# Performance work log

Measured on AMD Instinct MI355X. Metric: run time of the kernel, lower is better.

## Reference

```python
import jax, jax.numpy as jnp
import numpy as np

NUM_HEADS = 8
EMBED_DIM = 512
EXPAND = 3
RPE_DIM = 512
RPE_LAYERS = 3
B, N = 4, 2048
D1 = (EXPAND * EMBED_DIM) // NUM_HEADS * NUM_HEADS  # 1536
HEAD_DIM = D1 // NUM_HEADS  # 192


def srms(x):
    # SimpleRMSNorm: x / (||x||_2 * d^{-1/2} + eps)
    d = x.shape[-1]
    rms = jnp.linalg.norm(x, axis=-1, keepdims=True) * (d ** -0.5)
    return x / (rms + 1e-8)


def rpe_net(idx, Wp, bp, Wl, bl, Wr, br):
    # idx: (m, 1) relative positions -> (m, h*head_dim)
    h = idx @ Wp.T + bp
    for i in range(Wl.shape[0]):  # fixed small layer count
        h = jax.nn.relu(srms(h)) @ Wl[i].T + bl[i]
    return jax.nn.relu(srms(h)) @ Wr.T + br


def setup_inputs() -> dict:
    key = jax.random.key(0)
    ks = jax.random.split(key, 12)
    s = 0.02
    return {
        "x": jax.random.normal(ks[0], (B, N, EMBED_DIM), jnp.float32),
        "Wu": jax.random.normal(ks[1], (D1, EMBED_DIM), jnp.float32) * s,
        "bu": jnp.zeros((D1,), jnp.float32),
        "Wv": jax.random.normal(ks[2], (D1, EMBED_DIM), jnp.float32) * s,
        "bv": jnp.zeros((D1,), jnp.float32),
        "Wo": jax.random.normal(ks[3], (EMBED_DIM, D1), jnp.float32) * s,
        "bo": jnp.zeros((EMBED_DIM,), jnp.float32),
        "Wp": jax.random.normal(ks[4], (RPE_DIM, 1), jnp.float32) * s,
        "bp": jax.random.normal(ks[5], (RPE_DIM,), jnp.float32) * s,
        "Wl": jax.random.normal(ks[6], (RPE_LAYERS, RPE_DIM, RPE_DIM), jnp.float32) * s,
        "bl": jax.random.normal(ks[7], (RPE_LAYERS, RPE_DIM), jnp.float32) * s,
        "Wr": jax.random.normal(ks[8], (NUM_HEADS * HEAD_DIM, RPE_DIM), jnp.float32) * s,
        "br": jax.random.normal(ks[9], (NUM_HEADS * HEAD_DIM,), jnp.float32) * s,
    }


def reference(x, Wu, bu, Wv, bv, Wo, bo, Wp, bp, Wl, bl, Wr, br):
    b, n, e = x.shape
    d1 = Wu.shape[0]
    hd = d1 // NUM_HEADS
    u = jax.nn.silu(x @ Wu.T + bu)                       # (b, n, d1)
    v = jax.nn.silu(x @ Wv.T + bv)                       # (b, n, d1)
    v = v.reshape(b, n, NUM_HEADS, hd).transpose(0, 2, 1, 3)  # (b, h, n, d)
    # Tno non-causal, par_type=1: indices [0, 1..n-1, 0, -(n-1)..-1]
    pos = jnp.arange(1, n, dtype=x.dtype)
    zero = jnp.zeros((1,), x.dtype)
    idx = jnp.concatenate([zero, pos, zero, -pos[::-1]])[:, None]  # (2n, 1)
    a = rpe_net(idx, Wp, bp, Wl, bl, Wr, br)             # (2n, h*d)
    a = a.reshape(2 * n, NUM_HEADS, hd).transpose(1, 0, 2)  # (h, 2n, d)
    m = 2 * n
    # circular conv of length 2n along sequence, truncate to n
    y = jnp.fft.rfft(v, m, axis=2) * jnp.fft.rfft(a, m, axis=1)[None]
    out = jnp.fft.irfft(y, m, axis=2)[:, :, :n, :]       # (b, h, n, d)
    out = out.transpose(0, 2, 1, 3).reshape(b, n, d1)    # (b, n, d1)
    return (u * out) @ Wo.T + bo
```

## Files before the change

### kernel.cpp

```cpp
#include <hip/hip_runtime.h>

#define N_SEQ 2048
#define M_FFT 4096
#define D1    1536
#define NH    8
#define HD    192
#define ED    512

typedef __bf16 bf16;
typedef __bf16 bf16x4 __attribute__((ext_vector_type(4)));
typedef __bf16 bf16x8 __attribute__((ext_vector_type(8)));
typedef float  floatx4 __attribute__((ext_vector_type(4)));
typedef float  cx __attribute__((ext_vector_type(2)));

enum { MODE_PLAIN = 0, MODE_SILU_UV = 1, MODE_AT = 3, MODE_RPE = 4 };

__device__ __forceinline__ void gload16(const void* g, void* l) {
    __builtin_amdgcn_global_load_lds(
        (const __attribute__((address_space(1))) void*)g,
        (__attribute__((address_space(3))) void*)l, 16, 0, 0);
}

template<int MODE, typename OutT>
__global__ __launch_bounds__(256) void gemm_bf16(
    const bf16* __restrict__ A, const bf16* __restrict__ Bw,
    const float* __restrict__ bias, const float* __restrict__ bias2,
    OutT* __restrict__ C, OutT* __restrict__ C2,
    int M, int Nc, int K,
    const float* __restrict__ scale_in, float* __restrict__ sumsq_out)
{
    __shared__ __align__(16) bf16 As[128 * 32];
    __shared__ __align__(16) bf16 Bs[128 * 32];

    const int tid  = threadIdx.x;
    const int row0 = blockIdx.y * 128;
    const int col0 = blockIdx.x * 128;
    const int wid  = tid >> 6;
    const int lane = tid & 63;
    const int lm   = lane & 15;
    const int lk   = lane >> 4;
    const int wm   = wid >> 1;
    const int wn   = wid & 1;
    const int ldrow  = tid >> 2;
    const int ldcol8 = (tid & 3) * 8;

    floatx4 acc[4][4] = {};

    const bf16* Ag = A  + ((size_t)(row0 + ldrow)) * K + ldcol8;
    const bf16* Bg = Bw + ((size_t)(col0 + ldrow)) * K + ldcol8;
    bf16* AsW = As + (wid * 16) * 32;
    bf16* BsW = Bs + (wid * 16) * 32;

    for (int k0 = 0; k0 < K; k0 += 32) {
        gload16(Ag + k0, AsW);
        gload16(Ag + (size_t)64 * K + k0, AsW + 64 * 32);
        gload16(Bg + k0, BsW);
        gload16(Bg + (size_t)64 * K + k0, BsW + 64 * 32);
        __syncthreads();

        bf16x8 af[4], bfr[4];
        #pragma unroll
        for (int mi = 0; mi < 4; ++mi)
            af[mi] = *(const bf16x8*)&As[(wm * 64 + mi * 16 + lm) * 32 + lk * 8];
        #pragma unroll
        for (int nj = 0; nj < 4; ++nj)
            bfr[nj] = *(const bf16x8*)&Bs[(wn * 64 + nj * 16 + lm) * 32 + lk * 8];
        #pragma unroll
        for (int mi = 0; mi < 4; ++mi)
            #pragma unroll
            for (int nj = 0; nj < 4; ++nj)
                acc[mi][nj] = __builtin_amdgcn_mfma_f32_16x16x32_bf16(
                    af[mi], bfr[nj], acc[mi][nj], 0, 0, 0);
        __syncthreads();
    }

    const float* bs = bias;
    OutT* dst = C;
    int cadj = 0;
    if (MODE == MODE_SILU_UV && col0 >= D1) { bs = bias2; dst = C2; cadj = D1; }

    float bcol[4];
    #pragma unroll
    for (int nj = 0; nj < 4; ++nj)
        bcol[nj] = bs[col0 - cadj + wn * 64 + nj * 16 + lm];

    if (MODE == MODE_RPE) {
        #pragma unroll
        for (int mi = 0; mi < 4; ++mi) {
            #pragma unroll
            for (int r = 0; r < 4; ++r) {
                const int row = row0 + wm * 64 + mi * 16 + lk * 4 + r;
                float sc = 1.0f;
                if (scale_in)
                    sc = 1.0f / (sqrtf(scale_in[row]) * 0.04419417382415922f + 1e-8f);
                float ssq = 0.0f;
                #pragma unroll
                for (int nj = 0; nj < 4; ++nj) {
                    const int col = col0 + wn * 64 + nj * 16 + lm;
                    float val = acc[mi][nj][r] * sc + bcol[nj];
                    ssq += val * val;
                    ((bf16*)C)[(size_t)row * Nc + col] = (bf16)fmaxf(val, 0.0f);
                }
                ssq += __shfl_xor(ssq, 1, 64);
                ssq += __shfl_xor(ssq, 2, 64);
                ssq += __shfl_xor(ssq, 4, 64);
                ssq += __shfl_xor(ssq, 8, 64);
                if (lm == 0) atomicAdd(&sumsq_out[row], ssq);
            }
        }
        return;
    }

    #pragma unroll
    for (int mi = 0; mi < 4; ++mi) {
        const int rbase = row0 + wm * 64 + mi * 16 + lk * 4;
        float sc[4];
        #pragma unroll
        for (int r = 0; r < 4; ++r) {
            sc[r] = 1.0f;
            if (MODE == MODE_AT && scale_in)
                sc[r] = 1.0f / (sqrtf(scale_in[rbase + r]) * 0.04419417382415922f + 1e-8f);
        }
        #pragma unroll
        for (int nj = 0; nj < 4; ++nj) {
            const int col = col0 - cadj + wn * 64 + nj * 16 + lm;
            float vals[4];
            #pragma unroll
            for (int r = 0; r < 4; ++r) {
                float val = acc[mi][nj][r] * sc[r] + bcol[nj];
                if (MODE == MODE_SILU_UV)
                    val = val / (1.0f + __expf(-val));
                vals[r] = val;
            }
            if (MODE == MODE_SILU_UV) {
                int b = rbase >> 11, s = rbase & 2047;
                bf16x4 o;
                #pragma unroll
                for (int r = 0; r < 4; ++r) o[r] = (bf16)vals[r];
                *(bf16x4*)&((bf16*)dst)[((size_t)(b * D1 + col)) * N_SEQ + s] = o;
            } else if (MODE == MODE_AT) {
                float4 o = make_float4(vals[0], vals[1], vals[2], vals[3]);
                *(float4*)&((float*)C)[(size_t)col * M + rbase] = o;
            } else {
                #pragma unroll
                for (int r = 0; r < 4; ++r)
                    C[(size_t)(rbase + r) * Nc + col] = (OutT)vals[r];
            }
        }
    }
}

__global__ __launch_bounds__(256) void f2b_all_kernel(
    const float* __restrict__ x,  const float* __restrict__ s0,
    const float* __restrict__ s1, const float* __restrict__ s2,
    const float* __restrict__ s3, const float* __restrict__ s4,
    const float* __restrict__ Wp, const float* __restrict__ bp,
    bf16* __restrict__ x_bf, bf16* __restrict__ w_bf,
    float* __restrict__ sumsq, bf16* __restrict__ g0)
{
    const int bid = blockIdx.x;
    const int tid = threadIdx.x;
    __shared__ float red[4];

    if (bid < 7936) {
        const float* src;
        bf16* dst;
        size_t off;
        if (bid < 4096) {
            src = x; dst = x_bf; off = (size_t)bid * 1024;
        } else {
            int t = bid - 4096;
            int seg = t / 768;
            src = seg == 0 ? s0 : seg == 1 ? s1 : seg == 2 ? s2
                : seg == 3 ? s3 : s4;
            dst = w_bf + (size_t)seg * 786432;
            off = (size_t)(t % 768) * 1024;
        }
        size_t i = off + (size_t)tid * 4;
        float4 f = *(const float4*)(src + i);
        union { bf16 h[4]; short4 s; } u4;
        u4.h[0] = (bf16)f.x; u4.h[1] = (bf16)f.y;
        u4.h[2] = (bf16)f.z; u4.h[3] = (bf16)f.w;
        *(short4*)(dst + i) = u4.s;
    } else if (bid < 7948) {
        size_t i = (size_t)(bid - 7936) * 1024 + (size_t)tid * 4;
        *(float4*)(sumsq + i) = make_float4(0.f, 0.f, 0.f, 0.f);
    } else {
        const int j = bid - 7948;
        float idxv = (j < N_SEQ) ? (float)j
                                 : (j == N_SEQ ? 0.0f : (float)(j - 2 * N_SEQ));
        float h1 = idxv * Wp[tid] + bp[tid];
        float h2 = idxv * Wp[tid + 256] + bp[tid + 256];
        float ss = h1 * h1 + h2 * h2;
        #pragma unroll
        for (int off = 32; off > 0; off >>= 1) ss += __shfl_down(ss, off, 64);
        if ((tid & 63) == 0) red[tid >> 6] = ss;
        __syncthreads();
        float tot = red[0] + red[1] + red[2] + red[3];
        float scale = 1.0f / (sqrtf(tot) * 0.04419417382415922f + 1e-8f);
        g0[(size_t)j * ED + tid]       = (bf16)fmaxf(h1 * scale, 0.0f);
        g0[(size_t)j * ED + tid + 256] = (bf16)fmaxf(h2 * scale, 0.0f);
    }
}

#define FFT_LDS_SZ 4381
#define CC1 0.9238795325112867f
#define SS1 0.3826834323650898f
#define RR2 0.7071067811865476f

__device__ __forceinline__ int fpad(int i) { return i + (i >> 4) + 2 * (i >> 8); }

__device__ __forceinline__ cx mkcx(float a, float b) { cx r; r.x = a; r.y = b; return r; }
__device__ __forceinline__ cx cmul(cx a, cx b) {
    cx br = mkcx(-b.y, b.x);
    return a.xx * b + a.yy * br;
}
__device__ __forceinline__ cx cneg_i(cx a) { return mkcx(a.y, -a.x); }
__device__ __forceinline__ cx cpos_i(cx a) { return mkcx(-a.y, a.x); }
__host__ __device__ constexpr int brev4(int t) {
    return ((t & 1) << 3) | ((t & 2) << 1) | ((t & 4) >> 1) | ((t & 8) >> 3);
}

template<bool HZ>
__device__ __forceinline__ void fft16_dif_r4(cx x[16]) {
    const cx W1 = mkcx( CC1, -SS1);
    const cx W2 = mkcx( RR2, -RR2);
    const cx W3 = mkcx( SS1, -CC1);
    const cx W6 = mkcx(-RR2, -RR2);
    const cx W9 = mkcx(-CC1,  SS1);
    #pragma unroll
    for (int n = 0; n < 4; ++n) {
        cx A, B, C, D;
        if (HZ) { A = x[n]; C = x[n]; B = x[n + 4]; D = x[n + 4]; }
        else {
            A = x[n] + x[n + 8];      C = x[n] - x[n + 8];
            B = x[n + 4] + x[n + 12]; D = x[n + 4] - x[n + 12];
        }
        cx s = A - B;
        cx nid = cneg_i(D);
        cx m = C + nid;
        cx p = C - nid;
        x[n] = A + B;
        if (n == 0)      { x[4] = s;            x[8]  = m;           x[12] = p; }
        else if (n == 1) { x[5] = cmul(s, W2);  x[9]  = cmul(m, W1); x[13] = cmul(p, W3); }
        else if (n == 2) { x[6] = cneg_i(s);    x[10] = cmul(m, W2); x[14] = cmul(p, W6); }
        else             { x[7] = cmul(s, W6);  x[11] = cmul(m, W3); x[15] = cmul(p, W9); }
    }
    #pragma unroll
    for (int q = 0; q < 16; q += 4) {
        cx a = x[q], b = x[q + 1], c = x[q + 2], d = x[q + 3];
        cx a1 = a + c, c1 = a - c;
        cx b1 = b + d, d1 = cneg_i(b - d);
        x[q]     = a1 + b1;
        x[q + 1] = a1 - b1;
        x[q + 2] = c1 + d1;
        x[q + 3] = c1 - d1;
    }
}

template<bool HALF_OUT>
__device__ __forceinline__ void fft16_dit_inv_r4(cx x[16]) {
    const cx V1 = mkcx( CC1, SS1);
    const cx V2 = mkcx( RR2, RR2);
    const cx V3 = mkcx( SS1, CC1);
    const cx V6 = mkcx(-RR2, RR2);
    #pragma unroll
    for (int q = 0; q < 16; q += 4) {
        cx a = x[q], b = x[q + 1], c = x[q + 2], d = x[q + 3];
        cx a1 = a + b, b1 = a - b;
        cx c1 = c + d, d1 = c - d;
        cx t = cpos_i(d1);
        x[q]     = a1 + c1;
        x[q + 2] = a1 - c1;
        x[q + 1] = b1 + t;
        x[q + 3] = b1 - t;
    }
    #pragma unroll
    for (int n = 0; n < 4; ++n) {
        cx t1, t2;
        if (n == 0)      { t1 = x[4];             t2 = x[12]; }
        else if (n == 1) { t1 = cmul(x[5],  V2);  t2 = cmul(x[13], V2); }
        else if (n == 2) { t1 = cpos_i(x[6]);     t2 = cpos_i(x[14]); }
        else             { t1 = cmul(x[7],  V6);  t2 = cmul(x[15], V6); }
        cx P = x[n] + t1, Q = x[n] - t1;
        cx R = x[n + 8] + t2, S = x[n + 8] - t2;
        cx t, u;
        if (n == 0)      { t = R;            u = S; }
        else if (n == 1) { t = cmul(R, V1);  u = cmul(S, V1); }
        else if (n == 2) { t = cmul(R, V2);  u = cmul(S, V2); }
        else             { t = cmul(R, V3);  u = cmul(S, V3); }
        cx iu = cpos_i(u);
        x[n]     = P + t;
        x[n + 4] = Q + iu;
        if (!HALF_OUT) {
            x[n + 8]  = P - t;
            x[n + 12] = Q - iu;
        }
    }
}

__device__ __forceinline__ void stage_twiddle_tree(
    cx v[16], int j, float rden, float sgn)
{
    float s, c;
    __sincosf(sgn * 6.283185307179586f * (float)j * rden, &s, &c);
    cx w[16];
    w[1] = mkcx(c, s);
    w[2] = cmul(w[1], w[1]);
    w[3] = cmul(w[1], w[2]);
    w[4] = cmul(w[2], w[2]);
    w[5] = cmul(w[1], w[4]);
    w[6] = cmul(w[2], w[4]);
    w[7] = cmul(w[3], w[4]);
    w[8] = cmul(w[4], w[4]);
    #pragma unroll
    for (int t = 9; t < 16; ++t) w[t] = cmul(w[t - 8], w[8]);
    #pragma unroll
    for (int tau = 1; tau < 16; ++tau)
        v[brev4(tau)] = cmul(v[brev4(tau)], w[tau]);
}

template<bool HALF_ZERO>
__device__ void fft4096_fwd(cx* d, int tid)
{
    cx v[16];
    {
        const int j = tid;
        if (HALF_ZERO) {
            #pragma unroll
            for (int t = 0; t < 8; ++t) v[t] = d[fpad(j + (t << 8))];
            fft16_dif_r4<true>(v);
        } else {
            #pragma unroll
            for (int t = 0; t < 16; ++t) v[t] = d[fpad(j + (t << 8))];
            fft16_dif_r4<false>(v);
        }
        stage_twiddle_tree(v, j, 1.0f / 4096.0f, -1.0f);
        #pragma unroll
        for (int p = 0; p < 16; ++p) d[fpad(j + (p << 8))] = v[p];
    }
    __syncthreads();
    {
        const int base = ((tid >> 4) << 8) + (tid & 15);
        #pragma unroll
        for (int t = 0; t < 16; ++t) v[t] = d[fpad(base + (t << 4))];
        fft16_dif_r4<false>(v);
        stage_twiddle_tree(v, tid & 15, 1.0f / 256.0f, -1.0f);
        #pragma unroll
        for (int p = 0; p < 16; ++p) d[fpad(base + (p << 4))] = v[p];
    }
    __syncthreads();
    {
        const int base = tid << 4;
        #pragma unroll
        for (int t = 0; t < 16; ++t) v[t] = d[fpad(base + t)];
        fft16_dif_r4<false>(v);
        #pragma unroll
        for (int p = 0; p < 16; ++p) d[fpad(base + p)] = v[p];
    }
    __syncthreads();
}

__global__ __launch_bounds__(256) void fft_a_kernel(
    const float* __restrict__ a_t, cx* __restrict__ Wspec)
{
    __shared__ cx data[FFT_LDS_SZ];
    const int tid = threadIdx.x;
    const int h = blockIdx.x / 96, dp = blockIdx.x % 96;

    const float* r0 = a_t + ((size_t)(h * HD + 2 * dp)) * M_FFT;
    const float* r1 = r0 + M_FFT;

    for (int j = tid; j < 4096; j += 256) data[fpad(j)] = mkcx(r0[j], r1[j]);
    __syncthreads();
    fft4096_fwd<false>(data, tid);

    cx* outrow = Wspec + (size_t)blockIdx.x * 4096;
    for (int j = tid; j < 4096; j += 256) outrow[j] = data[fpad(j)];
}

__global__ __launch_bounds__(256) void fft_conv_kernel(
    const bf16* __restrict__ v_t, const cx* __restrict__ Wspec,
    const bf16* __restrict__ u_t, bf16* __restrict__ gated_t)
{
    __shared__ cx data[FFT_LDS_SZ];
    const int tid = threadIdx.x;
    const int bx = blockIdx.x;
    const int b  = bx / 768;
    const int r  = bx % 768;
    const int h  = r / 96, dp = r % 96;
    const int ch = h * HD + 2 * dp;

    const bf16* z0 = v_t + ((size_t)(b * D1 + ch)) * N_SEQ;
    const bf16* z1 = z0 + N_SEQ;

    {
        const int s = tid * 8;
        bf16x8 a0 = *(const bf16x8*)(z0 + s);
        bf16x8 a1 = *(const bf16x8*)(z1 + s);
        #pragma unroll
        for (int i = 0; i < 8; ++i)
            data[fpad(s + i)] = mkcx((float)a0[i], (float)a1[i]);
    }
    __syncthreads();

    fft4096_fwd<true>(data, tid);

    const cx* Wrow = Wspec + (size_t)r * 4096;
    cx v[16];
    {
        const int base = tid << 4;
        #pragma unroll
        for (int i = 0; i < 16; ++i) {
            const int p  = base + i;
            const int k  = __brev((unsigned)p) >> 20;
            const int km = (4096 - k) & 4095;
            const int p2 = __brev((unsigned)km) >> 20;
            cx Zk = data[fpad(p)];
            cx Zm = data[fpad(p2)];
            cx Wk = Wrow[p];
            cx Wm = Wrow[p2];
            cx V0 = 0.5f * (Zk + mkcx(Zm.x, -Zm.y));
            cx V1 = 0.5f * (mkcx(Zk.y, -Zk.x) + mkcx(Zm.y, Zm.x));
            cx A0 = 0.5f * (Wk + mkcx(Wm.x, -Wm.y));
            cx A1 = 0.5f * (mkcx(Wk.y, -Wk.x) + mkcx(Wm.y, Wm.x));
            cx P = cmul(V0, A0), Q = cmul(V1, A1);
            v[i] = P + cpos_i(Q);
        }
        __syncthreads();
        fft16_dit_inv_r4<false>(v);
        #pragma unroll
        for (int i = 0; i < 16; ++i) data[fpad(base + i)] = v[i];
    }
    __syncthreads();
    {
        const int base = ((tid >> 4) << 8) + (tid & 15);
        #pragma unroll
        for (int p = 0; p < 16; ++p) v[p] = data[fpad(base + (p << 4))];
        stage_twiddle_tree(v, tid & 15, 1.0f / 256.0f, 1.0f);
        fft16_dit_inv_r4<false>(v);
        #pragma unroll
        for (int t = 0; t < 16; ++t) data[fpad(base + (t << 4))] = v[t];
    }
    __syncthreads();
    {
        const int j = tid;
        #pragma unroll
        for (int p = 0; p < 16; ++p) v[p] = data[fpad(j + (p << 8))];
        stage_twiddle_tree(v, j, 1.0f / 4096.0f, 1.0f);
        fft16_dit_inv_r4<true>(v);
        #pragma unroll
        for (int t = 0; t < 8; ++t) data[fpad(j + (t << 8))] = v[t];
    }
    __syncthreads();

    const float inv_m = 1.0f / 4096.0f;
    const bf16* u0 = u_t + ((size_t)(b * D1 + ch)) * N_SEQ;
    const bf16* u1 = u0 + N_SEQ;
    bf16* g0 = gated_t + ((size_t)(b * D1 + ch)) * N_SEQ;
    bf16* g1 = g0 + N_SEQ;
    {
        const int t = tid * 8;
        bf16x8 ua = *(const bf16x8*)(u0 + t);
        bf16x8 ub = *(const bf16x8*)(u1 + t);
        bf16x8 oa, ob;
        #pragma unroll
        for (int i = 0; i < 8; ++i) {
            cx y = data[fpad(t + i)];
            oa[i] = (bf16)(y.x * inv_m * (float)ua[i]);
            ob[i] = (bf16)(y.y * inv_m * (float)ub[i]);
        }
        *(bf16x8*)(g0 + t) = oa;
        *(bf16x8*)(g1 + t) = ob;
    }
}

__global__ __launch_bounds__(256) void transpose_cs_kernel(
    const bf16* __restrict__ in, bf16* __restrict__ outp)
{
    __shared__ bf16 tile[64 * 68];
    const int c0 = blockIdx.x * 64;
    const int m0 = blockIdx.y * 64;
    const int b  = m0 >> 11;
    const int s0 = m0 & 2047;
    const int tid = threadIdx.x;
    const int cl = tid >> 4;
    const int sc = (tid & 15) * 4;
    #pragma unroll
    for (int p = 0; p < 4; ++p) {
        int c = p * 16 + cl;
        bf16x4 v = *(const bf16x4*)&in[((size_t)(b * D1 + c0 + c)) * N_SEQ + s0 + sc];
        *(bf16x4*)&tile[c * 68 + sc] = v;
    }
    __syncthreads();
    const int sl = tid >> 4;
    const int cc = (tid & 15) * 4;
    #pragma unroll
    for (int p = 0; p < 4; ++p) {
        int s = p * 16 + sl;
        bf16x4 o;
        #pragma unroll
        for (int j = 0; j < 4; ++j) o[j] = tile[(cc + j) * 68 + s];
        *(bf16x4*)&outp[((size_t)(m0 + s)) * D1 + c0 + cc] = o;
    }
}

extern "C" void kernel_launch(void* const* d_in, const int* in_sizes, int n_in,
                              void* d_out, int out_size, void* d_ws, size_t ws_size,
                              hipStream_t stream)
{
    const float* x  = (const float*)d_in[0];
    const float* Wu = (const float*)d_in[1];
    const float* bu = (const float*)d_in[2];
    const float* Wv = (const float*)d_in[3];
    const float* bv = (const float*)d_in[4];
    const float* Wo = (const float*)d_in[5];
    const float* bo = (const float*)d_in[6];
    const float* Wp = (const float*)d_in[7];
    const float* bp = (const float*)d_in[8];
    const float* Wl = (const float*)d_in[9];
    const float* bl = (const float*)d_in[10];
    const float* Wr = (const float*)d_in[11];
    const float* br = (const float*)d_in[12];
    float* out = (float*)d_out;

    float* ws      = (float*)d_ws;
    float* a_t     = ws;
    float* Wspec   = a_t   + 6291456;
    float* sumsq   = Wspec + 6291456;
    bf16*  bfws    = (bf16*)(sumsq + 12288);
    bf16*  x_bf    = bfws;
    bf16*  w_bf    = x_bf    + 4194304;
    bf16*  Wuv_bf  = w_bf;
    bf16*  Wo_bf   = w_bf    + 2 * 786432;
    bf16*  Wl_bf   = Wo_bf   + 786432;
    bf16*  Wr_bf   = Wl_bf   + 786432;
    bf16*  gA      = Wr_bf   + 786432;
    bf16*  gB      = gA      + 2097152;
    bf16*  u_t     = gB      + 2097152;
    bf16*  v_t     = u_t     + 12582912;
    bf16*  gated_t = v_t     + 12582912;
    bf16*  gated   = gated_t + 12582912;

    dim3 blk(256);

    f2b_all_kernel<<<4096 + 5 * 768 + 12 + 4096, blk, 0, stream>>>(
        x, Wu, Wv, Wo, Wl, Wr, Wp, bp, x_bf, w_bf, sumsq, gA);

    gemm_bf16<MODE_SILU_UV, bf16><<<dim3(24, 64), blk, 0, stream>>>(
        x_bf, Wuv_bf, bu, bv, u_t, v_t, 8192, 2 * D1, ED, nullptr, nullptr);

    bf16* gin = gA;
    bf16* gout = gB;
    for (int i = 0; i < 3; ++i) {
        const float* sin_p = (i == 0) ? nullptr : sumsq + (size_t)(i - 1) * 4096;
        gemm_bf16<MODE_RPE, bf16><<<dim3(4, 32), blk, 0, stream>>>(
            gin, Wl_bf + (size_t)i * ED * ED, bl + (size_t)i * ED, nullptr,
            gout, nullptr, 4096, ED, ED, sin_p, sumsq + (size_t)i * 4096);
        bf16* t = gin; gin = gout; gout = t;
    }
    gemm_bf16<MODE_AT, float><<<dim3(12, 32), blk, 0, stream>>>(
        gin, Wr_bf, br, nullptr, a_t, nullptr, 4096, D1, ED,
        sumsq + 2 * 4096, nullptr);

    fft_a_kernel<<<768, blk, 0, stream>>>(a_t, (cx*)Wspec);
    fft_conv_kernel<<<3072, blk, 0, stream>>>(
        v_t, (const cx*)Wspec, u_t, gated_t);

    transpose_cs_kernel<<<dim3(24, 128), blk, 0, stream>>>(gated_t, gated);

    gemm_bf16<MODE_PLAIN, float><<<dim3(4, 64), blk, 0, stream>>>(
        gated, Wo_bf, bo, nullptr, out, nullptr, 8192, ED, D1,
        nullptr, nullptr);
}
```

Before: 362.7 us.

## Precompute FFT twiddles and split kernel spectrum into A0/A1 halves once

Replaces the per-thread sincos plus twiddle-tree computation with a twiddle table built once in the setup kernel, which the FFT stages read from global memory. The kernel-side spectrum separation (A0/A1 from the packed two-channel FFT, with the 1/m and 1/2 scales folded in) moves into fft_a_kernel, so the conv kernel no longer recomputes it for every batch. Bit-reversed index math is replaced by simpler mask-based pairing, and LDS addressing uses constant strides. The cost is extra global reads of the twiddle table and of the two spectra, and a_t is overwritten in place to hold A1.

```diff
diff --git a/kernel.cpp b/kernel.cpp
--- a/kernel.cpp
+++ b/kernel.cpp
@@ -156,7 +156,8 @@
     const float* __restrict__ s3, const float* __restrict__ s4,
     const float* __restrict__ Wp, const float* __restrict__ bp,
     bf16* __restrict__ x_bf, bf16* __restrict__ w_bf,
-    float* __restrict__ sumsq, bf16* __restrict__ g0)
+    float* __restrict__ sumsq, bf16* __restrict__ g0,
+    float* __restrict__ twd)
 {
     const int bid = blockIdx.x;
     const int tid = threadIdx.x;
@@ -185,7 +186,7 @@
     } else if (bid < 7948) {
         size_t i = (size_t)(bid - 7936) * 1024 + (size_t)tid * 4;
         *(float4*)(sumsq + i) = make_float4(0.f, 0.f, 0.f, 0.f);
-    } else {
+    } else if (bid < 12044) {
         const int j = bid - 7948;
         float idxv = (j < N_SEQ) ? (float)j
                                  : (j == N_SEQ ? 0.0f : (float)(j - 2 * N_SEQ));
@@ -200,13 +201,18 @@
         float scale = 1.0f / (sqrtf(tot) * 0.04419417382415922f + 1e-8f);
         g0[(size_t)j * ED + tid]       = (bf16)fmaxf(h1 * scale, 0.0f);
         g0[(size_t)j * ED + tid + 256] = (bf16)fmaxf(h2 * scale, 0.0f);
+    } else {
+        const int idx = (bid - 12044) * 256 + tid;
+        const int j = idx >> 4, tau = idx & 15;
+        float sA, cA;
+        __sincosf(-6.283185307179586f * (float)(j * tau) * (1.0f / 4096.0f),
+                  &sA, &cA);
+        cx w; w.x = cA; w.y = sA;
+        ((cx*)twd)[idx] = w;
     }
 }
 
 #define FFT_LDS_SZ 4381
-#define CC1 0.9238795325112867f
-#define SS1 0.3826834323650898f
-#define RR2 0.7071067811865476f
 
 __device__ __forceinline__ int fpad(int i) { return i + (i >> 4) + 2 * (i >> 8); }
 
@@ -215,11 +221,20 @@
     cx br = mkcx(-b.y, b.x);
     return a.xx * b + a.yy * br;
 }
+__device__ __forceinline__ cx cmul_cj(cx a, cx b) {
+    cx bc = mkcx(b.x, -b.y);
+    cx br = mkcx(b.y, b.x);
+    return a.xx * bc + a.yy * br;
+}
 __device__ __forceinline__ cx cneg_i(cx a) { return mkcx(a.y, -a.x); }
 __device__ __forceinline__ cx cpos_i(cx a) { return mkcx(-a.y, a.x); }
 __host__ __device__ constexpr int brev4(int t) {
     return ((t & 1) << 3) | ((t & 2) << 1) | ((t & 4) >> 1) | ((t & 8) >> 3);
 }
+
+#define CC1 0.9238795325112867f
+#define SS1 0.3826834323650898f
+#define RR2 0.7071067811865476f
 
 template<bool HZ>
 __device__ __forceinline__ void fft16_dif_r4(cx x[16]) {
@@ -299,176 +314,219 @@
     }
 }
 
-__device__ __forceinline__ void stage_twiddle_tree(
-    cx v[16], int j, float rden, float sgn)
+template<bool CONJ>
+__device__ __forceinline__ void apply_tw(cx v[16], const cx tw[16]) {
+    #pragma unroll
+    for (int tau = 1; tau < 16; ++tau) {
+        const int q = brev4(tau);
+        v[q] = CONJ ? cmul_cj(v[q], tw[tau]) : cmul(v[q], tw[tau]);
+    }
+}
+
+template<bool HALF_ZERO>
+__device__ void fft4096_fwd(cx* d, int tid, const cx* __restrict__ Twd)
 {
-    float s, c;
-    __sincosf(sgn * 6.283185307179586f * (float)j * rden, &s, &c);
-    cx w[16];
-    w[1] = mkcx(c, s);
-    w[2] = cmul(w[1], w[1]);
-    w[3] = cmul(w[1], w[2]);
-    w[4] = cmul(w[2], w[2]);
-    w[5] = cmul(w[1], w[4]);
-    w[6] = cmul(w[2], w[4]);
-    w[7] = cmul(w[3], w[4]);
-    w[8] = cmul(w[4], w[4]);
-    #pragma unroll
-    for (int t = 9; t < 16; ++t) w[t] = cmul(w[t - 8], w[8]);
-    #pragma unroll
-    for (int tau = 1; tau < 16; ++tau)
-        v[brev4(tau)] = cmul(v[brev4(tau)], w[tau]);
-}
-
-template<bool HALF_ZERO>
-__device__ void fft4096_fwd(cx* d, int tid)
-{
-    cx v[16];
-    {
-        const int j = tid;
+    cx v[16], tw[16];
+    {
+        cx* base = d + fpad(tid);
+        const cx* Tr = Twd + (tid << 4);
+        #pragma unroll
+        for (int t = 1; t < 16; ++t) tw[t] = Tr[t];
         if (HALF_ZERO) {
             #pragma unroll
-            for (int t = 0; t < 8; ++t) v[t] = d[fpad(j + (t << 8))];
+            for (int t = 0; t < 8; ++t) v[t] = base[274 * t];
             fft16_dif_r4<true>(v);
         } else {
             #pragma unroll
-            for (int t = 0; t < 16; ++t) v[t] = d[fpad(j + (t << 8))];
+            for (int t = 0; t < 16; ++t) v[t] = base[274 * t];
             fft16_dif_r4<false>(v);
         }
-        stage_twiddle_tree(v, j, 1.0f / 4096.0f, -1.0f);
-        #pragma unroll
-        for (int p = 0; p < 16; ++p) d[fpad(j + (p << 8))] = v[p];
-    }
-    __syncthreads();
-    {
-        const int base = ((tid >> 4) << 8) + (tid & 15);
-        #pragma unroll
-        for (int t = 0; t < 16; ++t) v[t] = d[fpad(base + (t << 4))];
+        apply_tw<false>(v, tw);
+        #pragma unroll
+        for (int p = 0; p < 16; ++p) base[274 * p] = v[p];
+    }
+    __syncthreads();
+    {
+        cx* base = d + fpad(((tid >> 4) << 8) + (tid & 15));
+        const cx* Tr = Twd + ((tid & 15) << 8);
+        #pragma unroll
+        for (int t = 1; t < 16; ++t) tw[t] = Tr[t];
+        #pragma unroll
+        for (int t = 0; t < 16; ++t) v[t] = base[17 * t];
         fft16_dif_r4<false>(v);
-        stage_twiddle_tree(v, tid & 15, 1.0f / 256.0f, -1.0f);
-        #pragma unroll
-        for (int p = 0; p < 16; ++p) d[fpad(base + (p << 4))] = v[p];
-    }
-    __syncthreads();
-    {
-        const int base = tid << 4;
-        #pragma unroll
-        for (int t = 0; t < 16; ++t) v[t] = d[fpad(base + t)];
+        apply_tw<false>(v, tw);
+        #pragma unroll
+        for (int p = 0; p < 16; ++p) base[17 * p] = v[p];
+    }
+    __syncthreads();
+    {
+        cx* base = d + fpad(tid << 4);
+        #pragma unroll
+        for (int t = 0; t < 16; ++t) v[t] = base[t];
         fft16_dif_r4<false>(v);
         #pragma unroll
-        for (int p = 0; p < 16; ++p) d[fpad(base + p)] = v[p];
-    }
-    __syncthreads();
-}
-
-__global__ __launch_bounds__(256) void fft_a_kernel(
-    const float* __restrict__ a_t, cx* __restrict__ Wspec)
+        for (int p = 0; p < 16; ++p) base[p] = v[p];
+    }
+    __syncthreads();
+}
+
+__global__ __launch_bounds__(256, 4) void fft_a_kernel(
+    const float* a_t, cx* __restrict__ A0s, cx* A1s,
+    const cx* __restrict__ Twd)
 {
     __shared__ cx data[FFT_LDS_SZ];
     const int tid = threadIdx.x;
-    const int h = blockIdx.x / 96, dp = blockIdx.x % 96;
-
-    const float* r0 = a_t + ((size_t)(h * HD + 2 * dp)) * M_FFT;
+    const int r = blockIdx.x;
+
+    const float* r0 = a_t + (size_t)(2 * r) * M_FFT;
     const float* r1 = r0 + M_FFT;
-
-    for (int j = tid; j < 4096; j += 256) data[fpad(j)] = mkcx(r0[j], r1[j]);
-    __syncthreads();
-    fft4096_fwd<false>(data, tid);
-
-    cx* outrow = Wspec + (size_t)blockIdx.x * 4096;
-    for (int j = tid; j < 4096; j += 256) outrow[j] = data[fpad(j)];
-}
-
-__global__ __launch_bounds__(256) void fft_conv_kernel(
-    const bf16* __restrict__ v_t, const cx* __restrict__ Wspec,
-    const bf16* __restrict__ u_t, bf16* __restrict__ gated_t)
+    {
+        cx* base = data + fpad(tid);
+        #pragma unroll
+        for (int k = 0; k < 16; ++k)
+            base[274 * k] = mkcx(r0[tid + 256 * k], r1[tid + 256 * k]);
+    }
+    __syncthreads();
+    fft4096_fwd<false>(data, tid, Twd);
+
+    const float c = 0.25f / 4096.0f;
+    cx* A0row = A0s + (size_t)r * 4096;
+    cx* A1row = A1s + (size_t)r * 4096;
+    if (tid == 0) {
+        #pragma unroll
+        for (int i = 0; i < 16; ++i) {
+            const int p2 = (i < 2) ? i : (i ^ ((1 << (31 - __clz(i))) - 1));
+            cx Wk = data[fpad(i)];
+            cx Wm = data[fpad(p2)];
+            cx cjWm = mkcx(Wm.x, -Wm.y);
+            A0row[i] = c * (Wk + cjWm);
+            A1row[i] = c * cneg_i(Wk - cjWm);
+        }
+    } else {
+        const int base = tid << 4;
+        const int mask = (1 << (31 - __clz(base))) - 1;
+        const cx* zb  = data + fpad(base);
+        const cx* zb2 = data + fpad((base ^ mask) - 15);
+        #pragma unroll
+        for (int i = 0; i < 16; ++i) {
+            cx Wk = zb[i];
+            cx Wm = zb2[15 - i];
+            cx cjWm = mkcx(Wm.x, -Wm.y);
+            A0row[base + i] = c * (Wk + cjWm);
+            A1row[base + i] = c * cneg_i(Wk - cjWm);
+        }
+    }
+}
+
+__global__ __launch_bounds__(256, 4) void fft_conv_kernel(
+    const bf16* __restrict__ v_t, const cx* __restrict__ A0s,
+    const cx* __restrict__ A1s, const bf16* __restrict__ u_t,
+    bf16* __restrict__ gated_t, const cx* __restrict__ Twd)
 {
     __shared__ cx data[FFT_LDS_SZ];
     const int tid = threadIdx.x;
     const int bx = blockIdx.x;
     const int b  = bx / 768;
-    const int r  = bx % 768;
-    const int h  = r / 96, dp = r % 96;
-    const int ch = h * HD + 2 * dp;
+    const int r  = bx - b * 768;
+    const int ch = 2 * r;
 
     const bf16* z0 = v_t + ((size_t)(b * D1 + ch)) * N_SEQ;
     const bf16* z1 = z0 + N_SEQ;
 
     {
         const int s = tid * 8;
+        cx* base = data + fpad(s);
         bf16x8 a0 = *(const bf16x8*)(z0 + s);
         bf16x8 a1 = *(const bf16x8*)(z1 + s);
         #pragma unroll
         for (int i = 0; i < 8; ++i)
-            data[fpad(s + i)] = mkcx((float)a0[i], (float)a1[i]);
-    }
-    __syncthreads();
-
-    fft4096_fwd<true>(data, tid);
-
-    const cx* Wrow = Wspec + (size_t)r * 4096;
-    cx v[16];
-    {
-        const int base = tid << 4;
-        #pragma unroll
-        for (int i = 0; i < 16; ++i) {
-            const int p  = base + i;
-            const int k  = __brev((unsigned)p) >> 20;
-            const int km = (4096 - k) & 4095;
-            const int p2 = __brev((unsigned)km) >> 20;
-            cx Zk = data[fpad(p)];
-            cx Zm = data[fpad(p2)];
-            cx Wk = Wrow[p];
-            cx Wm = Wrow[p2];
-            cx V0 = 0.5f * (Zk + mkcx(Zm.x, -Zm.y));
-            cx V1 = 0.5f * (mkcx(Zk.y, -Zk.x) + mkcx(Zm.y, Zm.x));
-            cx A0 = 0.5f * (Wk + mkcx(Wm.x, -Wm.y));
-            cx A1 = 0.5f * (mkcx(Wk.y, -Wk.x) + mkcx(Wm.y, Wm.x));
-            cx P = cmul(V0, A0), Q = cmul(V1, A1);
-            v[i] = P + cpos_i(Q);
+            base[i] = mkcx((float)a0[i], (float)a1[i]);
+    }
+    __syncthreads();
+
+    fft4096_fwd<true>(data, tid, Twd);
+
+    cx v[16], tw[16];
+    const cx* A0row = A0s + (size_t)r * 4096;
+    const cx* A1row = A1s + (size_t)r * 4096;
+    const int pbase = tid << 4;
+    {
+        if (tid == 0) {
+            #pragma unroll
+            for (int i = 0; i < 16; ++i) {
+                const int p2 = (i < 2) ? i : (i ^ ((1 << (31 - __clz(i))) - 1));
+                cx Zk = data[fpad(i)];
+                cx Zm = data[fpad(p2)];
+                cx cjZm = mkcx(Zm.x, -Zm.y);
+                cx V0 = Zk + cjZm;
+                cx V1 = cneg_i(Zk - cjZm);
+                v[i] = cmul(V0, A0row[i]) + cpos_i(cmul(V1, A1row[i]));
+            }
+        } else {
+            const int mask = (1 << (31 - __clz(pbase))) - 1;
+            const cx* zb  = data + fpad(pbase);
+            const cx* zb2 = data + fpad((pbase ^ mask) - 15);
+            #pragma unroll
+            for (int i = 0; i < 16; ++i) {
+                cx Zk = zb[i];
+                cx Zm = zb2[15 - i];
+                cx a0 = A0row[pbase + i];
+                cx a1 = A1row[pbase + i];
+                cx cjZm = mkcx(Zm.x, -Zm.y);
+                cx V0 = Zk + cjZm;
+                cx V1 = cneg_i(Zk - cjZm);
+                v[i] = cmul(V0, a0) + cpos_i(cmul(V1, a1));
+            }
         }
         __syncthreads();
         fft16_dit_inv_r4<false>(v);
-        #pragma unroll
-        for (int i = 0; i < 16; ++i) data[fpad(base + i)] = v[i];
-    }
-    __syncthreads();
-    {
-        const int base = ((tid >> 4) << 8) + (tid & 15);
-        #pragma unroll
-        for (int p = 0; p < 16; ++p) v[p] = data[fpad(base + (p << 4))];
-        stage_twiddle_tree(v, tid & 15, 1.0f / 256.0f, 1.0f);
+        cx* base = data + fpad(pbase);
+        #pragma unroll
+        for (int i = 0; i < 16; ++i) base[i] = v[i];
+    }
+    __syncthreads();
+    {
+        cx* base = data + fpad(((tid >> 4) << 8) + (tid & 15));
+        const cx* Tr = Twd + ((tid & 15) << 8);
+        #pragma unroll
+        for (int t = 1; t < 16; ++t) tw[t] = Tr[t];
+        #pragma unroll
+        for (int p = 0; p < 16; ++p) v[p] = base[17 * p];
+        apply_tw<true>(v, tw);
         fft16_dit_inv_r4<false>(v);
         #pragma unroll
-        for (int t = 0; t < 16; ++t) data[fpad(base + (t << 4))] = v[t];
-    }
-    __syncthreads();
-    {
-        const int j = tid;
-        #pragma unroll
-        for (int p = 0; p < 16; ++p) v[p] = data[fpad(j + (p << 8))];
-        stage_twiddle_tree(v, j, 1.0f / 4096.0f, 1.0f);
+        for (int t = 0; t < 16; ++t) base[17 * t] = v[t];
+    }
+    __syncthreads();
+    {
+        cx* base = data + fpad(tid);
+        const cx* Tr = Twd + (tid << 4);
+        #pragma unroll
+        for (int t = 1; t < 16; ++t) tw[t] = Tr[t];
+        #pragma unroll
+        for (int p = 0; p < 16; ++p) v[p] = base[274 * p];
+        apply_tw<true>(v, tw);
         fft16_dit_inv_r4<true>(v);
         #pragma unroll
-        for (int t = 0; t < 8; ++t) data[fpad(j + (t << 8))] = v[t];
-    }
-    __syncthreads();
-
-    const float inv_m = 1.0f / 4096.0f;
+        for (int t = 0; t < 8; ++t) base[274 * t] = v[t];
+    }
+    __syncthreads();
+
     const bf16* u0 = u_t + ((size_t)(b * D1 + ch)) * N_SEQ;
     const bf16* u1 = u0 + N_SEQ;
     bf16* g0 = gated_t + ((size_t)(b * D1 + ch)) * N_SEQ;
     bf16* g1 = g0 + N_SEQ;
     {
         const int t = tid * 8;
+        const cx* base = data + fpad(t);
         bf16x8 ua = *(const bf16x8*)(u0 + t);
         bf16x8 ub = *(const bf16x8*)(u1 + t);
         bf16x8 oa, ob;
         #pragma unroll
         for (int i = 0; i < 8; ++i) {
-            cx y = data[fpad(t + i)];
-            oa[i] = (bf16)(y.x * inv_m * (float)ua[i]);
-            ob[i] = (bf16)(y.y * inv_m * (float)ub[i]);
+            cx y = base[i];
+            oa[i] = (bf16)(y.x * (float)ua[i]);
+            ob[i] = (bf16)(y.y * (float)ub[i]);
         }
         *(bf16x8*)(g0 + t) = oa;
         *(bf16x8*)(g1 + t) = ob;
@@ -526,9 +584,10 @@
 
     float* ws      = (float*)d_ws;
     float* a_t     = ws;
-    float* Wspec   = a_t   + 6291456;
-    float* sumsq   = Wspec + 6291456;
-    bf16*  bfws    = (bf16*)(sumsq + 12288);
+    float* A0spec  = a_t   + 6291456;
+    float* sumsq   = A0spec + 6291456;
+    float* twd     = sumsq + 12288;
+    bf16*  bfws    = (bf16*)(twd + 8192);
     bf16*  x_bf    = bfws;
     bf16*  w_bf    = x_bf    + 4194304;
     bf16*  Wuv_bf  = w_bf;
@@ -544,8 +603,8 @@
 
     dim3 blk(256);
 
-    f2b_all_kernel<<<4096 + 5 * 768 + 12 + 4096, blk, 0, stream>>>(
-        x, Wu, Wv, Wo, Wl, Wr, Wp, bp, x_bf, w_bf, sumsq, gA);
+    f2b_all_kernel<<<4096 + 5 * 768 + 12 + 4096 + 16, blk, 0, stream>>>(
+        x, Wu, Wv, Wo, Wl, Wr, Wp, bp, x_bf, w_bf, sumsq, gA, twd);
 
     gemm_bf16<MODE_SILU_UV, bf16><<<dim3(24, 64), blk, 0, stream>>>(
         x_bf, Wuv_bf, bu, bv, u_t, v_t, 8192, 2 * D1, ED, nullptr, nullptr);
@@ -563,9 +622,10 @@
         gin, Wr_bf, br, nullptr, a_t, nullptr, 4096, D1, ED,
         sumsq + 2 * 4096, nullptr);
 
-    fft_a_kernel<<<768, blk, 0, stream>>>(a_t, (cx*)Wspec);
+    fft_a_kernel<<<768, blk, 0, stream>>>(
+        a_t, (cx*)A0spec, (cx*)a_t, (const cx*)twd);
     fft_conv_kernel<<<3072, blk, 0, stream>>>(
-        v_t, (const cx*)Wspec, u_t, gated_t);
+        v_t, (const cx*)A0spec, (const cx*)a_t, u_t, gated_t, (const cx*)twd);
 
     transpose_cs_kernel<<<dim3(24, 128), blk, 0, stream>>>(gated_t, gated);
 
```

Measured after the change: 400.8 us. 1.1x slower.
